# Optimization experiments

Hardware: AMD Instinct MI355X
Metric: run time of the kernel (lower is better)

Reference implementation:

```python
import jax, jax.numpy as jnp
import numpy as np

DIM = 1024
NUM_HEADS = 16
HEAD_DIM = DIM // NUM_HEADS
SCALE = HEAD_DIM ** -0.5


def setup_inputs() -> dict:
    key = jax.random.key(0)
    ks = jax.random.split(key, 10)
    B, N, C = 8, 2048, DIM
    std = C ** -0.5
    return {
        "query": jax.random.normal(ks[0], (B, N, C), jnp.float32),
        "key": jax.random.normal(ks[1], (B, N, C), jnp.float32),
        "value": jax.random.normal(ks[2], (B, N, C), jnp.float32),
        "xpos": jax.random.randint(ks[3], (B, N, 2), 0, 64),
        "ypos": jax.random.randint(ks[4], (B, N, 2), 0, 64),
        # Linear weights stored [out, in] like torch; qkv_bias=False so no q/k/v bias.
        "Wq": jax.random.normal(ks[5], (C, C), jnp.float32) * std,
        "Wk": jax.random.normal(ks[6], (C, C), jnp.float32) * std,
        "Wv": jax.random.normal(ks[7], (C, C), jnp.float32) * std,
        "Wp": jax.random.normal(ks[8], (C, C), jnp.float32) * std,
        "bp": jax.random.normal(ks[9], (C,), jnp.float32) * std,
    }


def reference(query, key, value, xpos, ypos, Wq, Wk, Wv, Wp, bp):
    B, N, C = query.shape
    H, D = NUM_HEADS, HEAD_DIM
    # Separate Q/K/V projections (no bias), reshape to (B, N, H, D).
    q = (query @ Wq.T).reshape(B, N, H, D)
    k = (key @ Wk.T).reshape(B, N, H, D)
    v = (value @ Wv.T).reshape(B, N, H, D)
    # rope is None in this config, so no rotary embedding is applied.
    # Faithful to the source: NO permute before q @ k^T, so the contraction is
    # over D with attention logits of shape (B, N, H, H) (softmax over heads).
    attn = jnp.einsum("bnhd,bngd->bnhg", q, k) * SCALE
    attn = jax.nn.softmax(attn, axis=-1)
    x = jnp.einsum("bnhg,bngd->bnhd", attn, v)  # (B, N, H, D)
    # torch: (attn @ v).transpose(1, 2).reshape(B, N, C)
    x = jnp.transpose(x, (0, 2, 1, 3)).reshape(B, N, C)
    # Output projection (has bias); dropouts are p=0 / eval -> identity.
    return x @ Wp.T + bp
```

## Files before the change

### kernel.cpp

```cpp
#include <hip/hip_runtime.h>
#include <stdint.h>

#define DEV __device__ __forceinline__

using f32x4 = __attribute__((ext_vector_type(4))) float;
using s16x8 = __attribute__((ext_vector_type(8))) short;

DEV uint16_t f2bf(float f) {
  union { float f; uint32_t u; } v; v.f = f;
  uint32_t r = v.u + 0x7fffu + ((v.u >> 16) & 1u);
  return (uint16_t)(r >> 16);
}
DEV uint32_t pack2(float a, float b) {
  return (uint32_t)f2bf(a) | ((uint32_t)f2bf(b) << 16);
}

DEV void gload_lds16(const void* g, void* l) {
  __builtin_amdgcn_global_load_lds(
      (__attribute__((address_space(1))) void*)(void*)g,
      (__attribute__((address_space(3))) void*)l, 16, 0, 0);
}

__global__ __launch_bounds__(256) void cvt_w_kernel(const float* __restrict__ Wq,
                                                    const float* __restrict__ Wk,
                                                    const float* __restrict__ Wv,
                                                    const float* __restrict__ Wp,
                                                    uint16_t* __restrict__ wqb,
                                                    uint16_t* __restrict__ wkb,
                                                    uint16_t* __restrict__ wvb,
                                                    uint16_t* __restrict__ wpb) {
  const int idx = blockIdx.x * blockDim.x + threadIdx.x;
  const int region = idx >> 17;
  const int i = idx & 131071;
  const float* src = region == 0 ? Wq : region == 1 ? Wk : region == 2 ? Wv : Wp;
  uint16_t* dst = region == 0 ? wqb : region == 1 ? wkb : region == 2 ? wvb : wpb;
  const float4* s = (const float4*)src;
  float4 a = s[2 * i];
  float4 b = s[2 * i + 1];
  uint4 pk;
  pk.x = pack2(a.x, a.y);
  pk.y = pack2(a.z, a.w);
  pk.z = pack2(b.x, b.y);
  pk.w = pack2(b.z, b.w);
  ((uint4*)dst)[i] = pk;
}

struct GemmBatch {
  const void* A[3];
  const uint16_t* B[3];
  void* C[3];
};

template <bool A_F32, bool OUT_BF16>
__global__ __launch_bounds__(256) void gemm_bt(GemmBatch gb,
                                               const float* __restrict__ bias,
                                               int M, int N, int K) {
  constexpr int BM = 128, BN = 128, BK = 32;
  __shared__ __align__(16) uint16_t Alds[BM * BK];
  __shared__ __align__(16) uint16_t Blds[BN * BK];

  const int w = blockIdx.x;
  const int xcd = w & 7;
  int local = w >> 3;
  const int nbn = N >> 7;
  const int bmpx = (M >> 7) >> 3;
  const int bn = local % nbn;
  local /= nbn;
  const int bml = local % bmpx;
  const int z = local / bmpx;
  const int bm0 = (xcd * bmpx + bml) * BM;
  const int bn0 = bn * BN;

  const void* __restrict__ Ap = gb.A[z];
  const uint16_t* __restrict__ Bp = gb.B[z];
  void* __restrict__ Cp = gb.C[z];

  const int tid = threadIdx.x;
  const int wave = tid >> 6;
  const int lane = tid & 63;
  const int quad = lane >> 4;
  const int l16 = lane & 15;
  const int wm = (wave >> 1) * 64;
  const int wn = (wave & 1) * 64;

  f32x4 acc[4][4];
#pragma unroll
  for (int i = 0; i < 4; ++i)
#pragma unroll
    for (int j = 0; j < 4; ++j) acc[i][j] = (f32x4){0.f, 0.f, 0.f, 0.f};

  const uint16_t* bsrc[2];
  uint16_t* bdst[2];
#pragma unroll
  for (int j = 0; j < 2; ++j) {
    const int p = wave * 128 + j * 64 + lane;
    const int m = p >> 2;
    const int lc = (p & 3) ^ ((m >> 1) & 3);
    bsrc[j] = Bp + (size_t)(bn0 + m) * K + lc * 8;
    bdst[j] = &Blds[(wave * 128 + j * 64) * 8];
  }

  const float* asrcf[2];
  int adst_f[2];
  const uint16_t* asrc16[2];
  uint16_t* adst16[2];
  float4 cur[2][2], nxt[2][2];
  if constexpr (A_F32) {
#pragma unroll
    for (int c = 0; c < 2; ++c) {
      const int p = tid + c * 256;
      const int m = p >> 2;
      const int lc = (p & 3) ^ ((m >> 1) & 3);
      asrcf[c] = (const float*)Ap + (size_t)(bm0 + m) * K + lc * 8;
      adst_f[c] = p * 8;
    }
#pragma unroll
    for (int c = 0; c < 2; ++c) {
      const float4* g = (const float4*)asrcf[c];
      cur[c][0] = g[0];
      cur[c][1] = g[1];
    }
  } else {
#pragma unroll
    for (int j = 0; j < 2; ++j) {
      const int p = wave * 128 + j * 64 + lane;
      const int m = p >> 2;
      const int lc = (p & 3) ^ ((m >> 1) & 3);
      asrc16[j] = (const uint16_t*)Ap + (size_t)(bm0 + m) * K + lc * 8;
      adst16[j] = &Alds[(wave * 128 + j * 64) * 8];
    }
  }

  for (int k0 = 0; k0 < K; k0 += BK) {
#pragma unroll
    for (int j = 0; j < 2; ++j) gload_lds16(bsrc[j] + k0, bdst[j]);
    if constexpr (!A_F32) {
#pragma unroll
      for (int j = 0; j < 2; ++j) gload_lds16(asrc16[j] + k0, adst16[j]);
    } else {
#pragma unroll
      for (int c = 0; c < 2; ++c) {
        uint4 pk;
        pk.x = pack2(cur[c][0].x, cur[c][0].y);
        pk.y = pack2(cur[c][0].z, cur[c][0].w);
        pk.z = pack2(cur[c][1].x, cur[c][1].y);
        pk.w = pack2(cur[c][1].z, cur[c][1].w);
        *(uint4*)&Alds[adst_f[c]] = pk;
      }
      if (k0 + BK < K) {
#pragma unroll
        for (int c = 0; c < 2; ++c) {
          const float4* g = (const float4*)(asrcf[c] + k0 + BK);
          nxt[c][0] = g[0];
          nxt[c][1] = g[1];
        }
      }
    }
    __syncthreads();

    s16x8 af[4], bfv[4];
#pragma unroll
    for (int s = 0; s < 4; ++s) {
      const int ml = wm + s * 16 + l16;
      const int ca = ml * 4 + (quad ^ ((ml >> 1) & 3));
      af[s] = *(const s16x8*)&Alds[ca * 8];
      const int nl = wn + s * 16 + l16;
      const int cb = nl * 4 + (quad ^ ((nl >> 1) & 3));
      bfv[s] = *(const s16x8*)&Blds[cb * 8];
    }
#pragma unroll
    for (int sm = 0; sm < 4; ++sm)
#pragma unroll
      for (int sn = 0; sn < 4; ++sn)
        acc[sm][sn] =
            __builtin_amdgcn_mfma_f32_16x16x32_bf16(af[sm], bfv[sn], acc[sm][sn], 0, 0, 0);
    __syncthreads();

    if constexpr (A_F32) {
#pragma unroll
      for (int c = 0; c < 2; ++c) {
        cur[c][0] = nxt[c][0];
        cur[c][1] = nxt[c][1];
      }
    }
  }

#pragma unroll
  for (int sm = 0; sm < 4; ++sm) {
    const int mrow = bm0 + wm + sm * 16 + quad * 4;
#pragma unroll
    for (int sn = 0; sn < 4; ++sn) {
      const int ncol = bn0 + wn + sn * 16 + l16;
      if constexpr (OUT_BF16) {
        uint16_t* Cb = (uint16_t*)Cp;
#pragma unroll
        for (int r = 0; r < 4; ++r) Cb[(size_t)(mrow + r) * N + ncol] = f2bf(acc[sm][sn][r]);
      } else {
        float* Cf = (float*)Cp;
        const float bv = bias[ncol];
#pragma unroll
        for (int r = 0; r < 4; ++r) Cf[(size_t)(mrow + r) * N + ncol] = acc[sm][sn][r] + bv;
      }
    }
  }
}

__global__ __launch_bounds__(256) void attn_kernel(const uint16_t* __restrict__ qb,
                                                   const uint16_t* __restrict__ kb,
                                                   const uint16_t* __restrict__ vb,
                                                   uint16_t* __restrict__ x2b) {
  __shared__ __align__(16) uint16_t plds[4][16 * 16];
  __shared__ __align__(16) uint16_t vlds[4][16 * 64];

  const int tid = threadIdx.x;
  const int wave = tid >> 6;
  const int lane = tid & 63;
  const int quad = lane >> 4;
  const int l16 = lane & 15;
  const int token = blockIdx.x * 4 + wave;
  const int b = token >> 11;
  const int n = token & 2047;
  const size_t base = (size_t)token * 1024;

  {
    const uint16_t* vt = vb + base;
    uint16_t* vl = vlds[wave];
#pragma unroll
    for (int c2 = 0; c2 < 2; ++c2) {
      const int p = lane + c2 * 64;
      const int g = p >> 3;
      const int cc = p & 7;
      const int cs = cc ^ (2 * (g >> 3));
      *(uint4*)&vl[g * 64 + cs * 8] = *(const uint4*)&vt[p * 8];
    }
  }

  const uint16_t* qrow = qb + base + l16 * 64 + quad * 8;
  const uint16_t* krow = kb + base + l16 * 64 + quad * 8;
  s16x8 aq0 = *(const s16x8*)qrow;
  s16x8 aq1 = *(const s16x8*)(qrow + 32);
  s16x8 bk0 = *(const s16x8*)krow;
  s16x8 bk1 = *(const s16x8*)(krow + 32);
  f32x4 s = (f32x4){0.f, 0.f, 0.f, 0.f};
  s = __builtin_amdgcn_mfma_f32_16x16x32_bf16(aq0, bk0, s, 0, 0, 0);
  s = __builtin_amdgcn_mfma_f32_16x16x32_bf16(aq1, bk1, s, 0, 0, 0);

  float p[4];
#pragma unroll
  for (int r = 0; r < 4; ++r) {
    float v = s[r] * 0.125f;
    float mx = v;
#pragma unroll
    for (int off = 1; off < 16; off <<= 1) mx = fmaxf(mx, __shfl_xor(mx, off));
    float e = __expf(v - mx);
    float sum = e;
#pragma unroll
    for (int off = 1; off < 16; off <<= 1) sum += __shfl_xor(sum, off);
    p[r] = e / sum;
  }

  uint16_t* pb = plds[wave];
#pragma unroll
  for (int r = 0; r < 4; ++r) pb[(quad * 4 + r) * 16 + l16] = f2bf(p[r]);
  __syncthreads();
  s16x8 ap = (s16x8){0, 0, 0, 0, 0, 0, 0, 0};
  if (quad < 2) ap = *(const s16x8*)&pb[l16 * 16 + quad * 8];

  s16x8 bv[4];
#pragma unroll
  for (int c = 0; c < 4; ++c) bv[c] = (s16x8){0, 0, 0, 0, 0, 0, 0, 0};
  if (quad < 2) {
    const uint16_t* vl = vlds[wave];
#pragma unroll
    for (int c = 0; c < 4; ++c) {
      const int cc = c * 2 + (l16 >> 3);
      const int dlo = l16 & 7;
#pragma unroll
      for (int j = 0; j < 8; ++j) {
        const int g = quad * 8 + j;
        const int cs = cc ^ (2 * (g >> 3));
        bv[c][j] = (short)vl[g * 64 + cs * 8 + dlo];
      }
    }
  }

  f32x4 xacc[4];
#pragma unroll
  for (int c = 0; c < 4; ++c) {
    xacc[c] = (f32x4){0.f, 0.f, 0.f, 0.f};
    xacc[c] = __builtin_amdgcn_mfma_f32_16x16x32_bf16(ap, bv[c], xacc[c], 0, 0, 0);
  }

  uint16_t* xout =
      x2b + (size_t)b * (2048 * 1024) + (size_t)(n & 15) * 64 + (size_t)(n >> 4) * 1024;
#pragma unroll
  for (int c = 0; c < 4; ++c) {
    const int d = c * 16 + l16;
#pragma unroll
    for (int r = 0; r < 4; ++r) {
      const int h = quad * 4 + r;
      xout[(size_t)h * 128 * 1024 + d] = f2bf(xacc[c][r]);
    }
  }
}

extern "C" void kernel_launch(void* const* d_in, const int* in_sizes, int n_in,
                              void* d_out, int out_size, void* d_ws, size_t ws_size,
                              hipStream_t stream) {
  const float* query = (const float*)d_in[0];
  const float* key = (const float*)d_in[1];
  const float* value = (const float*)d_in[2];
  const float* Wq = (const float*)d_in[5];
  const float* Wk = (const float*)d_in[6];
  const float* Wv = (const float*)d_in[7];
  const float* Wp = (const float*)d_in[8];
  const float* bp = (const float*)d_in[9];
  float* out = (float*)d_out;

  const int C = 1024;
  const int M = 8 * 2048;
  const size_t MC = (size_t)M * C;

  uint16_t* ws = (uint16_t*)d_ws;
  uint16_t* qb = ws;
  uint16_t* kb = qb + MC;
  uint16_t* vb = kb + MC;
  uint16_t* x2b = vb + MC;
  uint16_t* wqb = x2b + MC;
  uint16_t* wkb = wqb + (size_t)C * C;
  uint16_t* wvb = wkb + (size_t)C * C;
  uint16_t* wpb = wvb + (size_t)C * C;

  cvt_w_kernel<<<dim3(4 * 131072 / 256), dim3(256), 0, stream>>>(Wq, Wk, Wv, Wp, wqb, wkb,
                                                                 wvb, wpb);

  GemmBatch qkv;
  qkv.A[0] = query;  qkv.B[0] = wqb;  qkv.C[0] = qb;
  qkv.A[1] = key;    qkv.B[1] = wkb;  qkv.C[1] = kb;
  qkv.A[2] = value;  qkv.B[2] = wvb;  qkv.C[2] = vb;
  gemm_bt<true, true><<<dim3((M / 128) * (C / 128) * 3), dim3(256), 0, stream>>>(
      qkv, nullptr, M, C, C);

  attn_kernel<<<dim3(M / 4), dim3(256), 0, stream>>>(qb, kb, vb, x2b);

  GemmBatch fin;
  fin.A[0] = x2b;  fin.B[0] = wpb;  fin.C[0] = out;
  fin.A[1] = x2b;  fin.B[1] = wpb;  fin.C[1] = out;
  fin.A[2] = x2b;  fin.B[2] = wpb;  fin.C[2] = out;
  gemm_bt<false, false><<<dim3((M / 128) * (C / 128)), dim3(256), 0, stream>>>(fin, bp, M,
                                                                               C, C);
}
```

Baseline: 477.3 us.

## Double-buffer GEMM LDS tiles to overlap global loads with MFMA compute

Allocates two LDS buffers each for the A and B tiles. The next K-tile's global loads (async LDS loads for bf16 operands, register prefetch for the fp32 A) are issued into the alternate buffer before the MFMAs on the current buffer run. This drops one of the two barriers per iteration and is meant to hide global-load latency behind compute. In exchange it doubles LDS use per block, which may reduce occupancy, and correctness relies on the async LDS loads having completed by the single remaining barrier.

```diff
diff --git a/kernel.cpp b/kernel.cpp
--- a/kernel.cpp
+++ b/kernel.cpp
@@ -56,8 +56,8 @@
                                                const float* __restrict__ bias,
                                                int M, int N, int K) {
   constexpr int BM = 128, BN = 128, BK = 32;
-  __shared__ __align__(16) uint16_t Alds[BM * BK];
-  __shared__ __align__(16) uint16_t Blds[BN * BK];
+  __shared__ __align__(16) uint16_t Alds[2][BM * BK];
+  __shared__ __align__(16) uint16_t Blds[2][BN * BK];
 
   const int w = blockIdx.x;
   const int xcd = w & 7;
@@ -90,21 +90,21 @@
     for (int j = 0; j < 4; ++j) acc[i][j] = (f32x4){0.f, 0.f, 0.f, 0.f};
 
   const uint16_t* bsrc[2];
-  uint16_t* bdst[2];
+  int bofs[2];
 #pragma unroll
   for (int j = 0; j < 2; ++j) {
     const int p = wave * 128 + j * 64 + lane;
     const int m = p >> 2;
     const int lc = (p & 3) ^ ((m >> 1) & 3);
     bsrc[j] = Bp + (size_t)(bn0 + m) * K + lc * 8;
-    bdst[j] = &Blds[(wave * 128 + j * 64) * 8];
+    bofs[j] = (wave * 128 + j * 64) * 8;
   }
 
   const float* asrcf[2];
   int adst_f[2];
   const uint16_t* asrc16[2];
-  uint16_t* adst16[2];
-  float4 cur[2][2], nxt[2][2];
+  int aofs16[2];
+  float4 areg[2][2];
   if constexpr (A_F32) {
 #pragma unroll
     for (int c = 0; c < 2; ++c) {
@@ -117,8 +117,8 @@
 #pragma unroll
     for (int c = 0; c < 2; ++c) {
       const float4* g = (const float4*)asrcf[c];
-      cur[c][0] = g[0];
-      cur[c][1] = g[1];
+      areg[c][0] = g[0];
+      areg[c][1] = g[1];
     }
   } else {
 #pragma unroll
@@ -127,46 +127,59 @@
       const int m = p >> 2;
       const int lc = (p & 3) ^ ((m >> 1) & 3);
       asrc16[j] = (const uint16_t*)Ap + (size_t)(bm0 + m) * K + lc * 8;
-      adst16[j] = &Alds[(wave * 128 + j * 64) * 8];
-    }
-  }
-
+      aofs16[j] = (wave * 128 + j * 64) * 8;
+    }
+  }
+
+#pragma unroll
+  for (int j = 0; j < 2; ++j) gload_lds16(bsrc[j], &Blds[0][bofs[j]]);
+  if constexpr (!A_F32) {
+#pragma unroll
+    for (int j = 0; j < 2; ++j) gload_lds16(asrc16[j], &Alds[0][aofs16[j]]);
+  } else {
+#pragma unroll
+    for (int c = 0; c < 2; ++c) {
+      uint4 pk;
+      pk.x = pack2(areg[c][0].x, areg[c][0].y);
+      pk.y = pack2(areg[c][0].z, areg[c][0].w);
+      pk.z = pack2(areg[c][1].x, areg[c][1].y);
+      pk.w = pack2(areg[c][1].z, areg[c][1].w);
+      *(uint4*)&Alds[0][adst_f[c]] = pk;
+    }
+  }
+  __syncthreads();
+
+  int buf = 0;
   for (int k0 = 0; k0 < K; k0 += BK) {
-#pragma unroll
-    for (int j = 0; j < 2; ++j) gload_lds16(bsrc[j] + k0, bdst[j]);
-    if constexpr (!A_F32) {
-#pragma unroll
-      for (int j = 0; j < 2; ++j) gload_lds16(asrc16[j] + k0, adst16[j]);
-    } else {
-#pragma unroll
-      for (int c = 0; c < 2; ++c) {
-        uint4 pk;
-        pk.x = pack2(cur[c][0].x, cur[c][0].y);
-        pk.y = pack2(cur[c][0].z, cur[c][0].w);
-        pk.z = pack2(cur[c][1].x, cur[c][1].y);
-        pk.w = pack2(cur[c][1].z, cur[c][1].w);
-        *(uint4*)&Alds[adst_f[c]] = pk;
-      }
-      if (k0 + BK < K) {
+    const bool hn = (k0 + BK < K);
+    const int nb = buf ^ 1;
+
+    if (hn) {
+#pragma unroll
+      for (int j = 0; j < 2; ++j) gload_lds16(bsrc[j] + k0 + BK, &Blds[nb][bofs[j]]);
+      if constexpr (A_F32) {
 #pragma unroll
         for (int c = 0; c < 2; ++c) {
           const float4* g = (const float4*)(asrcf[c] + k0 + BK);
-          nxt[c][0] = g[0];
-          nxt[c][1] = g[1];
+          areg[c][0] = g[0];
+          areg[c][1] = g[1];
         }
+      } else {
+#pragma unroll
+        for (int j = 0; j < 2; ++j)
+          gload_lds16(asrc16[j] + k0 + BK, &Alds[nb][aofs16[j]]);
       }
     }
-    __syncthreads();
 
     s16x8 af[4], bfv[4];
 #pragma unroll
     for (int s = 0; s < 4; ++s) {
       const int ml = wm + s * 16 + l16;
       const int ca = ml * 4 + (quad ^ ((ml >> 1) & 3));
-      af[s] = *(const s16x8*)&Alds[ca * 8];
+      af[s] = *(const s16x8*)&Alds[buf][ca * 8];
       const int nl = wn + s * 16 + l16;
       const int cb = nl * 4 + (quad ^ ((nl >> 1) & 3));
-      bfv[s] = *(const s16x8*)&Blds[cb * 8];
+      bfv[s] = *(const s16x8*)&Blds[buf][cb * 8];
     }
 #pragma unroll
     for (int sm = 0; sm < 4; ++sm)
@@ -174,14 +187,21 @@
       for (int sn = 0; sn < 4; ++sn)
         acc[sm][sn] =
             __builtin_amdgcn_mfma_f32_16x16x32_bf16(af[sm], bfv[sn], acc[sm][sn], 0, 0, 0);
-    __syncthreads();
-
-    if constexpr (A_F32) {
-#pragma unroll
-      for (int c = 0; c < 2; ++c) {
-        cur[c][0] = nxt[c][0];
-        cur[c][1] = nxt[c][1];
+
+    if (hn) {
+      if constexpr (A_F32) {
+#pragma unroll
+        for (int c = 0; c < 2; ++c) {
+          uint4 pk;
+          pk.x = pack2(areg[c][0].x, areg[c][0].y);
+          pk.y = pack2(areg[c][0].z, areg[c][0].w);
+          pk.z = pack2(areg[c][1].x, areg[c][1].y);
+          pk.w = pack2(areg[c][1].z, areg[c][1].w);
+          *(uint4*)&Alds[nb][adst_f[c]] = pk;
+        }
       }
+      __syncthreads();
+      buf = nb;
     }
   }
 
```

New measurement: 620.0 us. 1.3x slower.

## Pre-convert fp32 activations to bf16 and load GEMM A via direct LDS

Applied to the files above, without the earlier changes.

Activations q/k/v are now converted to bf16 in a separate bulk pass together with the weights, instead of being converted inside the QKV GEMM. The GEMM then drops its fp32 register path and loads both A and B tiles with async global-to-LDS loads. The goal is a simpler, better-pipelined GEMM main loop that reads half as many A bytes. The cost is an extra full read and write of the activations (about 100MB of traffic) in the conversion kernel, plus a larger workspace.

```diff
diff --git a/kernel.cpp b/kernel.cpp
--- a/kernel.cpp
+++ b/kernel.cpp
@@ -21,19 +21,30 @@
       (__attribute__((address_space(3))) void*)l, 16, 0, 0);
 }
 
-__global__ __launch_bounds__(256) void cvt_w_kernel(const float* __restrict__ Wq,
-                                                    const float* __restrict__ Wk,
-                                                    const float* __restrict__ Wv,
-                                                    const float* __restrict__ Wp,
-                                                    uint16_t* __restrict__ wqb,
-                                                    uint16_t* __restrict__ wkb,
-                                                    uint16_t* __restrict__ wvb,
-                                                    uint16_t* __restrict__ wpb) {
+__global__ __launch_bounds__(256) void cvt_all_kernel(
+    const float* __restrict__ q, const float* __restrict__ k,
+    const float* __restrict__ v, const float* __restrict__ Wq,
+    const float* __restrict__ Wk, const float* __restrict__ Wv,
+    const float* __restrict__ Wp, uint16_t* __restrict__ qc,
+    uint16_t* __restrict__ kc, uint16_t* __restrict__ vc,
+    uint16_t* __restrict__ wqb, uint16_t* __restrict__ wkb,
+    uint16_t* __restrict__ wvb, uint16_t* __restrict__ wpb) {
   const int idx = blockIdx.x * blockDim.x + threadIdx.x;
-  const int region = idx >> 17;
-  const int i = idx & 131071;
-  const float* src = region == 0 ? Wq : region == 1 ? Wk : region == 2 ? Wv : Wp;
-  uint16_t* dst = region == 0 ? wqb : region == 1 ? wkb : region == 2 ? wvb : wpb;
+  const float* src;
+  uint16_t* dst;
+  int i;
+  if (idx < 3 * 2097152) {
+    const int t = idx >> 21;
+    i = idx & 2097151;
+    src = t == 0 ? q : t == 1 ? k : v;
+    dst = t == 0 ? qc : t == 1 ? kc : vc;
+  } else {
+    const int j = idx - 3 * 2097152;
+    const int r = j >> 17;
+    i = j & 131071;
+    src = r == 0 ? Wq : r == 1 ? Wk : r == 2 ? Wv : Wp;
+    dst = r == 0 ? wqb : r == 1 ? wkb : r == 2 ? wvb : wpb;
+  }
   const float4* s = (const float4*)src;
   float4 a = s[2 * i];
   float4 b = s[2 * i + 1];
@@ -46,12 +57,12 @@
 }
 
 struct GemmBatch {
-  const void* A[3];
+  const uint16_t* A[3];
   const uint16_t* B[3];
   void* C[3];
 };
 
-template <bool A_F32, bool OUT_BF16>
+template <bool OUT_BF16>
 __global__ __launch_bounds__(256) void gemm_bt(GemmBatch gb,
                                                const float* __restrict__ bias,
                                                int M, int N, int K) {
@@ -71,7 +82,7 @@
   const int bm0 = (xcd * bmpx + bml) * BM;
   const int bn0 = bn * BN;
 
-  const void* __restrict__ Ap = gb.A[z];
+  const uint16_t* __restrict__ Ap = gb.A[z];
   const uint16_t* __restrict__ Bp = gb.B[z];
   void* __restrict__ Cp = gb.C[z];
 
@@ -89,73 +100,26 @@
 #pragma unroll
     for (int j = 0; j < 4; ++j) acc[i][j] = (f32x4){0.f, 0.f, 0.f, 0.f};
 
+  const uint16_t* asrc[2];
   const uint16_t* bsrc[2];
+  uint16_t* adst[2];
   uint16_t* bdst[2];
 #pragma unroll
   for (int j = 0; j < 2; ++j) {
     const int p = wave * 128 + j * 64 + lane;
     const int m = p >> 2;
     const int lc = (p & 3) ^ ((m >> 1) & 3);
+    asrc[j] = Ap + (size_t)(bm0 + m) * K + lc * 8;
     bsrc[j] = Bp + (size_t)(bn0 + m) * K + lc * 8;
+    adst[j] = &Alds[(wave * 128 + j * 64) * 8];
     bdst[j] = &Blds[(wave * 128 + j * 64) * 8];
   }
 
-  const float* asrcf[2];
-  int adst_f[2];
-  const uint16_t* asrc16[2];
-  uint16_t* adst16[2];
-  float4 cur[2][2], nxt[2][2];
-  if constexpr (A_F32) {
-#pragma unroll
-    for (int c = 0; c < 2; ++c) {
-      const int p = tid + c * 256;
-      const int m = p >> 2;
-      const int lc = (p & 3) ^ ((m >> 1) & 3);
-      asrcf[c] = (const float*)Ap + (size_t)(bm0 + m) * K + lc * 8;
-      adst_f[c] = p * 8;
-    }
-#pragma unroll
-    for (int c = 0; c < 2; ++c) {
-      const float4* g = (const float4*)asrcf[c];
-      cur[c][0] = g[0];
-      cur[c][1] = g[1];
-    }
-  } else {
-#pragma unroll
-    for (int j = 0; j < 2; ++j) {
-      const int p = wave * 128 + j * 64 + lane;
-      const int m = p >> 2;
-      const int lc = (p & 3) ^ ((m >> 1) & 3);
-      asrc16[j] = (const uint16_t*)Ap + (size_t)(bm0 + m) * K + lc * 8;
-      adst16[j] = &Alds[(wave * 128 + j * 64) * 8];
-    }
-  }
-
   for (int k0 = 0; k0 < K; k0 += BK) {
 #pragma unroll
     for (int j = 0; j < 2; ++j) gload_lds16(bsrc[j] + k0, bdst[j]);
-    if constexpr (!A_F32) {
-#pragma unroll
-      for (int j = 0; j < 2; ++j) gload_lds16(asrc16[j] + k0, adst16[j]);
-    } else {
-#pragma unroll
-      for (int c = 0; c < 2; ++c) {
-        uint4 pk;
-        pk.x = pack2(cur[c][0].x, cur[c][0].y);
-        pk.y = pack2(cur[c][0].z, cur[c][0].w);
-        pk.z = pack2(cur[c][1].x, cur[c][1].y);
-        pk.w = pack2(cur[c][1].z, cur[c][1].w);
-        *(uint4*)&Alds[adst_f[c]] = pk;
-      }
-      if (k0 + BK < K) {
-#pragma unroll
-        for (int c = 0; c < 2; ++c) {
-          const float4* g = (const float4*)(asrcf[c] + k0 + BK);
-          nxt[c][0] = g[0];
-          nxt[c][1] = g[1];
-        }
-      }
-    }
+#pragma unroll
+    for (int j = 0; j < 2; ++j) gload_lds16(asrc[j] + k0, adst[j]);
     __syncthreads();
 
     s16x8 af[4], bfv[4];
@@ -175,14 +139,6 @@
         acc[sm][sn] =
             __builtin_amdgcn_mfma_f32_16x16x32_bf16(af[sm], bfv[sn], acc[sm][sn], 0, 0, 0);
     __syncthreads();
-
-    if constexpr (A_F32) {
-#pragma unroll
-      for (int c = 0; c < 2; ++c) {
-        cur[c][0] = nxt[c][0];
-        cur[c][1] = nxt[c][1];
-      }
-    }
   }
 
 #pragma unroll
@@ -320,6 +276,7 @@
   const int C = 1024;
   const int M = 8 * 2048;
   const size_t MC = (size_t)M * C;
+  const size_t CC = (size_t)C * C;
 
   uint16_t* ws = (uint16_t*)d_ws;
   uint16_t* qb = ws;
@@ -327,19 +284,22 @@
   uint16_t* vb = kb + MC;
   uint16_t* x2b = vb + MC;
   uint16_t* wqb = x2b + MC;
-  uint16_t* wkb = wqb + (size_t)C * C;
-  uint16_t* wvb = wkb + (size_t)C * C;
-  uint16_t* wpb = wvb + (size_t)C * C;
-
-  cvt_w_kernel<<<dim3(4 * 131072 / 256), dim3(256), 0, stream>>>(Wq, Wk, Wv, Wp, wqb, wkb,
-                                                                 wvb, wpb);
+  uint16_t* wkb = wqb + CC;
+  uint16_t* wvb = wkb + CC;
+  uint16_t* wpb = wvb + CC;
+  uint16_t* kin = wpb + CC;
+  uint16_t* vin = kin + MC;
+  uint16_t* qin = x2b;
+
+  cvt_all_kernel<<<dim3(26624), dim3(256), 0, stream>>>(
+      query, key, value, Wq, Wk, Wv, Wp, qin, kin, vin, wqb, wkb, wvb, wpb);
 
   GemmBatch qkv;
-  qkv.A[0] = query;  qkv.B[0] = wqb;  qkv.C[0] = qb;
-  qkv.A[1] = key;    qkv.B[1] = wkb;  qkv.C[1] = kb;
-  qkv.A[2] = value;  qkv.B[2] = wvb;  qkv.C[2] = vb;
-  gemm_bt<true, true><<<dim3((M / 128) * (C / 128) * 3), dim3(256), 0, stream>>>(
-      qkv, nullptr, M, C, C);
+  qkv.A[0] = qin;  qkv.B[0] = wqb;  qkv.C[0] = qb;
+  qkv.A[1] = kin;  qkv.B[1] = wkb;  qkv.C[1] = kb;
+  qkv.A[2] = vin;  qkv.B[2] = wvb;  qkv.C[2] = vb;
+  gemm_bt<true><<<dim3((M / 128) * (C / 128) * 3), dim3(256), 0, stream>>>(qkv, nullptr,
+                                                                           M, C, C);
 
   attn_kernel<<<dim3(M / 4), dim3(256), 0, stream>>>(qb, kb, vb, x2b);
 
@@ -347,6 +307,5 @@
   fin.A[0] = x2b;  fin.B[0] = wpb;  fin.C[0] = out;
   fin.A[1] = x2b;  fin.B[1] = wpb;  fin.C[1] = out;
   fin.A[2] = x2b;  fin.B[2] = wpb;  fin.C[2] = out;
-  gemm_bt<false, false><<<dim3((M / 128) * (C / 128)), dim3(256), 0, stream>>>(fin, bp, M,
-                                                                               C, C);
-}
+  gemm_bt<false><<<dim3((M / 128) * (C / 128)), dim3(256), 0, stream>>>(fin, bp, M, C, C);
+}
```

Result: faster. 448.3 us (-6.1%).
